# Optimization experiments

Hardware: AMD Instinct MI355X
Metric: run time of the kernel (lower is better)

## Reference

```python
import jax, jax.numpy as jnp
import numpy as np

TAU = 2.0          # LIFNode default
V_TH = 1.0         # threshold
V_RESET = 0.0      # hard reset value
SG_ALPHA = 4.0     # surrogate sigmoid alpha

@jax.custom_vjp
def spike_fn(u):
    # heaviside(u) with sigmoid surrogate gradient (spikingjelly default)
    return (u >= 0.0).astype(u.dtype)

def _spike_fwd(u):
    return spike_fn(u), u

def _spike_bwd(u, g):
    s = jax.nn.sigmoid(SG_ALPHA * u)
    return (g * SG_ALPHA * s * (1.0 - s),)

spike_fn.defvjp(_spike_fwd, _spike_bwd)

def lif_multistep(x_seq):
    # x_seq: [T, B, Cc]; hard-reset LIF, decay_input=True, v_reset=0
    def step(v, x_t):
        v = v + (x_t - (v - V_RESET)) / TAU   # charge
        s = spike_fn(v - V_TH)                # fire
        v = s * V_RESET + (1.0 - s) * v       # hard reset
        return v, s
    v0 = jnp.zeros_like(x_seq[0])
    _, spikes = jax.lax.scan(step, v0, x_seq)
    return spikes  # [T, B, Cc]

def setup_inputs() -> dict:
    key = jax.random.key(0)
    k1, k2, k3, k4 = jax.random.split(key, 4)
    T, B, C, H, Wd, Cc = 16, 16, 256, 32, 32, 256
    x = jax.random.normal(k1, (T, B, C, H, Wd), dtype=jnp.float32)
    condition = jax.random.normal(k2, (T, B, Cc), dtype=jnp.float32)
    W = jax.random.normal(k3, (2 * C, Cc), dtype=jnp.float32) * (1.0 / np.sqrt(Cc))
    b = jax.random.normal(k4, (2 * C,), dtype=jnp.float32) * 0.01
    return {"x": x, "condition": condition, "W": W, "b": b}

def reference(x, condition, W, b):
    T, B, C, H, Wd = x.shape
    spikes = lif_multistep(condition)                       # [T,B,Cc]
    params = jnp.einsum('tbc,dc->tbd', spikes, W) + b       # [T,B,2C]
    gamma, beta = jnp.split(params, 2, axis=2)              # each [T,B,C]
    gamma = gamma.reshape(T, B, C, 1, 1)
    beta = beta.reshape(T, B, C, 1, 1)
    return gamma * x + beta + x
```

## Files before the change

kernel.cpp:

```cpp
#include <hip/hip_runtime.h>


#define T_STEPS 16
#define B_SZ    16
#define C_SZ    256
#define CC_SZ   256
#define HW      1024
#define SLICES  32
#define THREADS 256

__global__ __launch_bounds__(THREADS, 8)
void film_fused_kernel(const float* __restrict__ x,
                       const float* __restrict__ cond,
                       const float* __restrict__ W,
                       const float* __restrict__ bias,
                       float* __restrict__ out)
{
    __shared__ float s_spk[CC_SZ];
    __shared__ float s_part[THREADS];
    __shared__ float s_g[SLICES];
    __shared__ float s_b[SLICES];

    const int bid   = blockIdx.x;
    const int tb    = bid >> 3;
    const int t     = tb >> 4;
    const int b     = tb & (B_SZ - 1);
    const int cbase = (bid & 7) * SLICES;
    const int tid   = threadIdx.x;

    const size_t x_base = ((size_t)tb * C_SZ + cbase) * HW;
    const float4* __restrict__ x4 = reinterpret_cast<const float4*>(x + x_base);
    float4*       __restrict__ o4 = reinterpret_cast<float4*>(out + x_base);
    float4 pf0 = x4[0 * 256 + tid];
    float4 pf1 = x4[1 * 256 + tid];
    float4 pf2 = x4[2 * 256 + tid];
    float4 pf3 = x4[3 * 256 + tid];

    {
        float v = 0.0f, s = 0.0f;
        const float* cp = cond + (size_t)b * CC_SZ + tid;
        for (int tt = 0; tt <= t; ++tt) {
            float xv = cp[(size_t)tt * (B_SZ * CC_SZ)];
            v = v + (xv - v) * 0.5f;
            s = ((v - 1.0f) >= 0.0f) ? 1.0f : 0.0f;
            v = (s != 0.0f) ? 0.0f : v;
        }
        s_spk[tid] = s;
    }
    __syncthreads();

    {
        const int r = tid >> 2;
        const int q = tid & 3;
        const int d = (r < 32) ? (cbase + r) : (C_SZ + cbase + (r - 32));
        const float4* Wr = reinterpret_cast<const float4*>(W + (size_t)d * CC_SZ)
                           + q * 16;
        const float* sp = s_spk + q * 64;
        float acc = 0.0f;
#pragma unroll
        for (int k = 0; k < 16; ++k) {
            float4 w = Wr[k];
            acc += w.x * sp[k * 4 + 0];
            acc += w.y * sp[k * 4 + 1];
            acc += w.z * sp[k * 4 + 2];
            acc += w.w * sp[k * 4 + 3];
        }
        s_part[tid] = acc;
    }
    __syncthreads();
    if (tid < 64) {
        const int r = tid;
        const int d = (r < 32) ? (cbase + r) : (C_SZ + cbase + (r - 32));
        float val = s_part[4 * r] + s_part[4 * r + 1]
                  + s_part[4 * r + 2] + s_part[4 * r + 3] + bias[d];
        if (r < 32) s_g[r] = val + 1.0f;
        else        s_b[r - 32] = val;
    }
    __syncthreads();

    {
        float4 r;
        float g, be;
        g = s_g[0]; be = s_b[0];
        r.x = fmaf(g, pf0.x, be); r.y = fmaf(g, pf0.y, be);
        r.z = fmaf(g, pf0.z, be); r.w = fmaf(g, pf0.w, be);
        o4[0 * 256 + tid] = r;
        g = s_g[1]; be = s_b[1];
        r.x = fmaf(g, pf1.x, be); r.y = fmaf(g, pf1.y, be);
        r.z = fmaf(g, pf1.z, be); r.w = fmaf(g, pf1.w, be);
        o4[1 * 256 + tid] = r;
        g = s_g[2]; be = s_b[2];
        r.x = fmaf(g, pf2.x, be); r.y = fmaf(g, pf2.y, be);
        r.z = fmaf(g, pf2.z, be); r.w = fmaf(g, pf2.w, be);
        o4[2 * 256 + tid] = r;
        g = s_g[3]; be = s_b[3];
        r.x = fmaf(g, pf3.x, be); r.y = fmaf(g, pf3.y, be);
        r.z = fmaf(g, pf3.z, be); r.w = fmaf(g, pf3.w, be);
        o4[3 * 256 + tid] = r;

#pragma unroll 4
        for (int sidx = 4; sidx < SLICES; ++sidx) {
            float4 v = x4[(size_t)sidx * 256 + tid];
            float gg = s_g[sidx], bb = s_b[sidx];
            float4 rr;
            rr.x = fmaf(gg, v.x, bb);
            rr.y = fmaf(gg, v.y, bb);
            rr.z = fmaf(gg, v.z, bb);
            rr.w = fmaf(gg, v.w, bb);
            o4[(size_t)sidx * 256 + tid] = rr;
        }
    }
}

extern "C" void kernel_launch(void* const* d_in, const int* in_sizes, int n_in,
                              void* d_out, int out_size, void* d_ws, size_t ws_size,
                              hipStream_t stream)
{
    const float* x    = (const float*)d_in[0];
    const float* cond = (const float*)d_in[1];
    const float* W    = (const float*)d_in[2];
    const float* bias = (const float*)d_in[3];
    float* out = (float*)d_out;

    film_fused_kernel<<<2048, THREADS, 0, stream>>>(x, cond, W, bias, out);
}
```

Baseline: 114.3 us.

## Use nontemporal loads/stores, software-pipeline streaming loop, shuffle-reduce GEMV

```diff
diff --git a/kernel.cpp b/kernel.cpp
--- a/kernel.cpp
+++ b/kernel.cpp
@@ -9,6 +9,8 @@
 #define SLICES  32
 #define THREADS 256
 
+typedef float f4 __attribute__((ext_vector_type(4)));
+
 __global__ __launch_bounds__(THREADS, 8)
 void film_fused_kernel(const float* __restrict__ x,
                        const float* __restrict__ cond,
@@ -17,7 +19,6 @@
                        float* __restrict__ out)
 {
     __shared__ float s_spk[CC_SZ];
-    __shared__ float s_part[THREADS];
     __shared__ float s_g[SLICES];
     __shared__ float s_b[SLICES];
 
@@ -29,21 +30,28 @@
     const int tid   = threadIdx.x;
 
     const size_t x_base = ((size_t)tb * C_SZ + cbase) * HW;
-    const float4* __restrict__ x4 = reinterpret_cast<const float4*>(x + x_base);
-    float4*       __restrict__ o4 = reinterpret_cast<float4*>(out + x_base);
-    float4 pf0 = x4[0 * 256 + tid];
-    float4 pf1 = x4[1 * 256 + tid];
-    float4 pf2 = x4[2 * 256 + tid];
-    float4 pf3 = x4[3 * 256 + tid];
+    const f4* __restrict__ x4 = reinterpret_cast<const f4*>(x + x_base);
+    f4*       __restrict__ o4 = reinterpret_cast<f4*>(out + x_base);
+
+    f4 pf0 = __builtin_nontemporal_load(&x4[0 * 256 + tid]);
+    f4 pf1 = __builtin_nontemporal_load(&x4[1 * 256 + tid]);
+    f4 pf2 = __builtin_nontemporal_load(&x4[2 * 256 + tid]);
+    f4 pf3 = __builtin_nontemporal_load(&x4[3 * 256 + tid]);
 
     {
+        const float* cp = cond + (size_t)b * CC_SZ + tid;
+        float cv[T_STEPS];
+#pragma unroll
+        for (int tt = 0; tt < T_STEPS; ++tt)
+            cv[tt] = cp[(size_t)tt * (B_SZ * CC_SZ)];
         float v = 0.0f, s = 0.0f;
-        const float* cp = cond + (size_t)b * CC_SZ + tid;
-        for (int tt = 0; tt <= t; ++tt) {
-            float xv = cp[(size_t)tt * (B_SZ * CC_SZ)];
-            v = v + (xv - v) * 0.5f;
-            s = ((v - 1.0f) >= 0.0f) ? 1.0f : 0.0f;
-            v = (s != 0.0f) ? 0.0f : v;
+#pragma unroll
+        for (int tt = 0; tt < T_STEPS; ++tt) {
+            if (tt <= t) {
+                v = v + (cv[tt] - v) * 0.5f;
+                s = (v >= 1.0f) ? 1.0f : 0.0f;
+                v = (s != 0.0f) ? 0.0f : v;
+            }
         }
         s_spk[tid] = s;
     }
@@ -53,63 +61,57 @@
         const int r = tid >> 2;
         const int q = tid & 3;
         const int d = (r < 32) ? (cbase + r) : (C_SZ + cbase + (r - 32));
-        const float4* Wr = reinterpret_cast<const float4*>(W + (size_t)d * CC_SZ)
-                           + q * 16;
+        const f4* Wr = reinterpret_cast<const f4*>(W + (size_t)d * CC_SZ)
+                       + q * 16;
         const float* sp = s_spk + q * 64;
         float acc = 0.0f;
 #pragma unroll
         for (int k = 0; k < 16; ++k) {
-            float4 w = Wr[k];
-            acc += w.x * sp[k * 4 + 0];
-            acc += w.y * sp[k * 4 + 1];
-            acc += w.z * sp[k * 4 + 2];
-            acc += w.w * sp[k * 4 + 3];
+            f4 w = Wr[k];
+            acc += w.x * sp[4 * k + 0];
+            acc += w.y * sp[4 * k + 1];
+            acc += w.z * sp[4 * k + 2];
+            acc += w.w * sp[4 * k + 3];
         }
-        s_part[tid] = acc;
-    }
-    __syncthreads();
-    if (tid < 64) {
-        const int r = tid;
-        const int d = (r < 32) ? (cbase + r) : (C_SZ + cbase + (r - 32));
-        float val = s_part[4 * r] + s_part[4 * r + 1]
-                  + s_part[4 * r + 2] + s_part[4 * r + 3] + bias[d];
-        if (r < 32) s_g[r] = val + 1.0f;
-        else        s_b[r - 32] = val;
+        acc += __shfl_xor(acc, 1);
+        acc += __shfl_xor(acc, 2);
+        if (q == 0) {
+            float val = acc + bias[d];
+            if (r < 32) s_g[r] = val + 1.0f;
+            else        s_b[r - 32] = val;
+        }
     }
     __syncthreads();
 
-    {
-        float4 r;
-        float g, be;
-        g = s_g[0]; be = s_b[0];
-        r.x = fmaf(g, pf0.x, be); r.y = fmaf(g, pf0.y, be);
-        r.z = fmaf(g, pf0.z, be); r.w = fmaf(g, pf0.w, be);
-        o4[0 * 256 + tid] = r;
-        g = s_g[1]; be = s_b[1];
-        r.x = fmaf(g, pf1.x, be); r.y = fmaf(g, pf1.y, be);
-        r.z = fmaf(g, pf1.z, be); r.w = fmaf(g, pf1.w, be);
-        o4[1 * 256 + tid] = r;
-        g = s_g[2]; be = s_b[2];
-        r.x = fmaf(g, pf2.x, be); r.y = fmaf(g, pf2.y, be);
-        r.z = fmaf(g, pf2.z, be); r.w = fmaf(g, pf2.w, be);
-        o4[2 * 256 + tid] = r;
-        g = s_g[3]; be = s_b[3];
-        r.x = fmaf(g, pf3.x, be); r.y = fmaf(g, pf3.y, be);
-        r.z = fmaf(g, pf3.z, be); r.w = fmaf(g, pf3.w, be);
-        o4[3 * 256 + tid] = r;
+#define APPLY_STORE(cc, so)                                                   \
+    {                                                                         \
+        float g_ = s_g[so], b_ = s_b[so];                                     \
+        f4 r_;                                                                \
+        r_.x = fmaf(g_, (cc).x, b_);                                          \
+        r_.y = fmaf(g_, (cc).y, b_);                                          \
+        r_.z = fmaf(g_, (cc).z, b_);                                          \
+        r_.w = fmaf(g_, (cc).w, b_);                                          \
+        __builtin_nontemporal_store(r_, &o4[(size_t)(so) * 256 + tid]);       \
+    }
 
-#pragma unroll 4
-        for (int sidx = 4; sidx < SLICES; ++sidx) {
-            float4 v = x4[(size_t)sidx * 256 + tid];
-            float gg = s_g[sidx], bb = s_b[sidx];
-            float4 rr;
-            rr.x = fmaf(gg, v.x, bb);
-            rr.y = fmaf(gg, v.y, bb);
-            rr.z = fmaf(gg, v.z, bb);
-            rr.w = fmaf(gg, v.w, bb);
-            o4[(size_t)sidx * 256 + tid] = rr;
-        }
+    f4 c0 = pf0, c1 = pf1, c2 = pf2, c3 = pf3;
+    int sidx = 0;
+    for (; sidx + 4 < SLICES; sidx += 4) {
+        f4 n0 = __builtin_nontemporal_load(&x4[(size_t)(sidx + 4) * 256 + tid]);
+        f4 n1 = __builtin_nontemporal_load(&x4[(size_t)(sidx + 5) * 256 + tid]);
+        f4 n2 = __builtin_nontemporal_load(&x4[(size_t)(sidx + 6) * 256 + tid]);
+        f4 n3 = __builtin_nontemporal_load(&x4[(size_t)(sidx + 7) * 256 + tid]);
+        APPLY_STORE(c0, sidx + 0);
+        APPLY_STORE(c1, sidx + 1);
+        APPLY_STORE(c2, sidx + 2);
+        APPLY_STORE(c3, sidx + 3);
+        c0 = n0; c1 = n1; c2 = n2; c3 = n3;
     }
+    APPLY_STORE(c0, sidx + 0);
+    APPLY_STORE(c1, sidx + 1);
+    APPLY_STORE(c2, sidx + 2);
+    APPLY_STORE(c3, sidx + 3);
+#undef APPLY_STORE
 }
 
 extern "C" void kernel_launch(void* const* d_in, const int* in_sizes, int n_in,
```

After: 105.6 us. 7.6% less time.
